# Optimization experiments

Hardware: AMD Instinct MI355X
Metric: run time of the kernel (lower is better)

Reference implementation:

```python
import jax, jax.numpy as jnp
import numpy as np

B, C, H, W = 8, 32, 256, 256


def setup_inputs() -> dict:
    key = jax.random.key(0)
    ks = jax.random.split(key, 9)
    x = jax.random.normal(ks[0], (B, C, H, W), dtype=jnp.float32)
    # depthwise 1x1 conv (groups=C) == per-channel scalar weight + bias
    def wb(kw, kb):
        w = jax.random.normal(kw, (C,), dtype=jnp.float32) * (1.0 / jnp.sqrt(1.0))
        b = jax.random.normal(kb, (C,), dtype=jnp.float32) * 0.1
        return w, b
    w_up, b_up = wb(ks[1], ks[2])
    w_right, b_right = wb(ks[3], ks[4])
    w_down, b_down = wb(ks[5], ks[6])
    w_left, b_left = wb(ks[7], ks[8])
    return {"x": x, "w_up": w_up, "b_up": b_up, "w_right": w_right,
            "b_right": b_right, "w_down": w_down, "b_down": b_down,
            "w_left": w_left, "b_left": b_left}


def _dir_scan(x_seq, w, b):
    """x_seq: [L, B, C, K]. h[0]=x[0]; h[t+1]=relu(w_c*h[t]+b_c+x[t+1])."""
    wb_ = w[None, :, None]
    bb_ = b[None, :, None]

    def step(h, xt):
        hn = jax.nn.relu(h * wb_ + bb_ + xt)
        return hn, hn

    _, ys = jax.lax.scan(step, x_seq[0], x_seq[1:])
    return jnp.concatenate([x_seq[:1], ys], axis=0)


def reference(x, w_up, b_up, w_right, b_right, w_down, b_down, w_left, b_left):
    xh = jnp.moveaxis(x, 2, 0)  # [H, B, C, W] for row scans
    xw = jnp.moveaxis(x, 3, 0)  # [W, B, C, H] for column scans

    top_down = jnp.moveaxis(_dir_scan(xh, w_down, b_down), 0, 2)
    top_up = jnp.moveaxis(_dir_scan(xh[::-1], w_up, b_up)[::-1], 0, 2)
    top_right = jnp.moveaxis(_dir_scan(xw, w_right, b_right), 0, 3)
    top_left = jnp.moveaxis(_dir_scan(xw[::-1], w_left, b_left)[::-1], 0, 3)

    return (top_up, top_right, top_down, top_left)
```

## Files before the change

### kernel.cpp

```cpp
#include <hip/hip_runtime.h>

#define BB 8
#define CC 32
#define HH 256
#define WW 256

__device__ __forceinline__ float step_v8(float h, float w, float b, float x) {
    float t = __fadd_rn(__fadd_rn(__fmul_rn(h, w), b), x);
    float r;
    asm volatile(
        "v_max_f32 %0, %1, 0\n\t"
        "v_min_f32 %0, %0, %2"
        : "=&v"(r)
        : "v"(t), "v"(3.3895313892515355e+38f));
    return r;
}

__global__ __launch_bounds__(256, 4) void irnn_fused_v8(
    const float* __restrict__ x,
    const float* __restrict__ w_up,    const float* __restrict__ b_up,
    const float* __restrict__ w_right, const float* __restrict__ b_right,
    const float* __restrict__ w_down,  const float* __restrict__ b_down,
    const float* __restrict__ w_left,  const float* __restrict__ b_left,
    float* __restrict__ out_up, float* __restrict__ out_right,
    float* __restrict__ out_down, float* __restrict__ out_left)
{
    __shared__ float tile[128 * 67];

    const int bid = blockIdx.x;
    if (bid < BB * CC) {
        const int bc   = bid;
        const int c    = bc & (CC - 1);
        const int down = (threadIdx.x < 128);
        const int t    = threadIdx.x & 127;
        const int w2   = t * 2;
        const float wc = down ? w_down[c] : w_up[c];
        const float bv = down ? b_down[c] : b_up[c];

        const long long base = (long long)bc * (HH * WW) + w2;
        const long long st   = down ? WW : -WW;
        const long long off0 = down ? 0 : (long long)(HH - 1) * WW;
        const float* xs = x + base + off0;
        float*       os = (down ? out_down : out_up) + base + off0;

        float2 h = *(const float2*)xs;
        *(float2*)os = h;

        float2 buf[8];
        #pragma unroll
        for (int i = 0; i < 8; ++i) buf[i] = *(const float2*)(xs + (1 + i) * st);

        int kb = 1;
        #pragma unroll 1
        for (int g = 0; g < 30; ++g) {
            float2 nb[8];
            #pragma unroll
            for (int i = 0; i < 8; ++i) nb[i] = *(const float2*)(xs + (kb + 8 + i) * st);
            #pragma unroll
            for (int i = 0; i < 8; ++i) {
                h.x = step_v8(h.x, wc, bv, buf[i].x);
                h.y = step_v8(h.y, wc, bv, buf[i].y);
                *(float2*)(os + (kb + i) * st) = h;
            }
            #pragma unroll
            for (int i = 0; i < 8; ++i) buf[i] = nb[i];
            kb += 8;
        }
        float2 tb[7];
        #pragma unroll
        for (int i = 0; i < 7; ++i) tb[i] = *(const float2*)(xs + (249 + i) * st);
        #pragma unroll
        for (int i = 0; i < 8; ++i) {
            h.x = step_v8(h.x, wc, bv, buf[i].x);
            h.y = step_v8(h.y, wc, bv, buf[i].y);
            *(float2*)(os + (241 + i) * st) = h;
        }
        #pragma unroll
        for (int i = 0; i < 7; ++i) {
            h.x = step_v8(h.x, wc, bv, tb[i].x);
            h.y = step_v8(h.y, wc, bv, tb[i].y);
            *(float2*)(os + (249 + i) * st) = h;
        }
        return;
    }

    const int hb  = bid - BB * CC;
    const int dir = hb & 1;
    const int rg  = hb >> 1;
    const int tid = threadIdx.x;
    const long long R0 = (long long)rg * 128;
    const int c = (int)((R0 >> 8) & (CC - 1));
    const float wc = dir ? w_left[c] : w_right[c];
    const float bv = dir ? b_left[c] : b_right[c];
    const float* xbase = x + R0 * WW;
    float* obase = (dir ? out_left : out_right) + R0 * WW;

    float h = 0.0f;
    for (int s = 0; s < 4; ++s) {
        const int tt = dir ? (3 - s) : s;
        const int w0 = tt * 64;

        #pragma unroll
        for (int it = 0; it < 8; ++it) {
            int idx = it * 256 + tid;
            int row = idx >> 4;
            int l   = idx & 15;
            float4 v = *(const float4*)(xbase + row * WW + w0 + l * 4);
            int a = row * 67 + l * 4;
            tile[a]     = v.x;
            tile[a + 1] = v.y;
            tile[a + 2] = v.z;
            tile[a + 3] = v.w;
        }
        __syncthreads();

        if (tid < 128) {
            float* trow = &tile[tid * 67];
            if (dir == 0) {
                float rb[16];
                #pragma unroll
                for (int i = 0; i < 16; ++i) rb[i] = trow[i];
                #pragma unroll
                for (int q = 0; q < 4; ++q) {
                    float nb[16];
                    if (q < 3) {
                        #pragma unroll
                        for (int i = 0; i < 16; ++i) nb[i] = trow[16 * (q + 1) + i];
                    }
                    #pragma unroll
                    for (int i = 0; i < 16; ++i) {
                        if (s == 0 && q == 0 && i == 0) h = rb[0];
                        else h = step_v8(h, wc, bv, rb[i]);
                        trow[16 * q + i] = h;
                    }
                    if (q < 3) {
                        #pragma unroll
                        for (int i = 0; i < 16; ++i) rb[i] = nb[i];
                    }
                }
            } else {
                float rb[16];
                #pragma unroll
                for (int i = 0; i < 16; ++i) rb[i] = trow[48 + i];
                #pragma unroll
                for (int q = 3; q >= 0; --q) {
                    float nb[16];
                    if (q > 0) {
                        #pragma unroll
                        for (int i = 0; i < 16; ++i) nb[i] = trow[16 * (q - 1) + i];
                    }
                    #pragma unroll
                    for (int i = 15; i >= 0; --i) {
                        if (s == 0 && q == 3 && i == 15) h = rb[15];
                        else h = step_v8(h, wc, bv, rb[i]);
                        trow[16 * q + i] = h;
                    }
                    if (q > 0) {
                        #pragma unroll
                        for (int i = 0; i < 16; ++i) rb[i] = nb[i];
                    }
                }
            }
        }
        __syncthreads();

        #pragma unroll
        for (int it = 0; it < 8; ++it) {
            int idx = it * 256 + tid;
            int row = idx >> 4;
            int l   = idx & 15;
            int a = row * 67 + l * 4;
            float4 v = make_float4(tile[a], tile[a + 1], tile[a + 2], tile[a + 3]);
            *(float4*)(obase + row * WW + w0 + l * 4) = v;
        }
        __syncthreads();
    }
}

extern "C" void kernel_launch(void* const* d_in, const int* in_sizes, int n_in,
                              void* d_out, int out_size, void* d_ws, size_t ws_size,
                              hipStream_t stream) {
    const float* x       = (const float*)d_in[0];
    const float* w_up    = (const float*)d_in[1];
    const float* b_up    = (const float*)d_in[2];
    const float* w_right = (const float*)d_in[3];
    const float* b_right = (const float*)d_in[4];
    const float* w_down  = (const float*)d_in[5];
    const float* b_down  = (const float*)d_in[6];
    const float* w_left  = (const float*)d_in[7];
    const float* b_left  = (const float*)d_in[8];

    float* out = (float*)d_out;
    const long long N = (long long)BB * CC * HH * WW;
    float* out_up    = out;
    float* out_right = out + N;
    float* out_down  = out + 2 * N;
    float* out_left  = out + 3 * N;

    irnn_fused_v8<<<dim3(BB * CC + 1024), 256, 0, stream>>>(
        x, w_up, b_up, w_right, b_right, w_down, b_down, w_left, b_left,
        out_up, out_right, out_down, out_left);
}
```

Measured before the change: 339.3 us.

## Restructure row-scan blocks with register-prefetch pipeline, interleaved roles, and nontemporal stores

Row-scan blocks now handle a whole 256-row image each, with all 256 threads scanning, in 8 column tiles of width 32. The next tile's global loads are prefetched into registers while the current tile is scanned, which removes one barrier per tile. Blocks are interleaved so column and row roles for the same (b,c) plane are launched adjacently in a 768-block grid. The step becomes an FMA plus a single med3 clamp instead of mul/add/add/max/min, and outputs use nontemporal stores. This trades larger per-block work and changed rounding (fma) for fewer blocks and less barrier overhead.

```diff
diff --git a/kernel.cpp b/kernel.cpp
--- a/kernel.cpp
+++ b/kernel.cpp
@@ -5,18 +5,21 @@
 #define HH 256
 #define WW 256
 
-__device__ __forceinline__ float step_v8(float h, float w, float b, float x) {
-    float t = __fadd_rn(__fadd_rn(__fmul_rn(h, w), b), x);
+typedef float vf2 __attribute__((ext_vector_type(2)));
+typedef float vf4 __attribute__((ext_vector_type(4)));
+
+__device__ __forceinline__ float step_v9(float h, float w, float bx) {
+    float t = __fmaf_rn(h, w, bx);
     float r;
-    asm volatile(
-        "v_max_f32 %0, %1, 0\n\t"
-        "v_min_f32 %0, %0, %2"
-        : "=&v"(r)
-        : "v"(t), "v"(3.3895313892515355e+38f));
+    asm volatile("v_med3_f32 %0, %1, 0, %2"
+                 : "=v"(r)
+                 : "v"(t), "v"(3.3895313892515355e+38f));
     return r;
 }
 
-__global__ __launch_bounds__(256, 4) void irnn_fused_v8(
+#define LDS_BARRIER() asm volatile("s_waitcnt lgkmcnt(0)\n\ts_barrier" ::: "memory")
+
+__global__ __launch_bounds__(256, 4) void irnn_fused_v9(
     const float* __restrict__ x,
     const float* __restrict__ w_up,    const float* __restrict__ b_up,
     const float* __restrict__ w_right, const float* __restrict__ b_right,
@@ -25,12 +28,17 @@
     float* __restrict__ out_up, float* __restrict__ out_right,
     float* __restrict__ out_down, float* __restrict__ out_left)
 {
-    __shared__ float tile[128 * 67];
-
-    const int bid = blockIdx.x;
-    if (bid < BB * CC) {
-        const int bc   = bid;
-        const int c    = bc & (CC - 1);
+    __shared__ float tile[256 * 33];
+
+    const int p    = blockIdx.x;
+    const int x8   = p & 7;
+    const int slot = p >> 3;
+    const int pg   = slot / 3;
+    const int role = slot - pg * 3;
+    const int bc   = pg * 8 + x8;
+    const int c    = bc & (CC - 1);
+
+    if (role == 0) {
         const int down = (threadIdx.x < 128);
         const int t    = threadIdx.x & 127;
         const int w2   = t * 2;
@@ -43,137 +51,151 @@
         const float* xs = x + base + off0;
         float*       os = (down ? out_down : out_up) + base + off0;
 
-        float2 h = *(const float2*)xs;
-        *(float2*)os = h;
-
-        float2 buf[8];
-        #pragma unroll
-        for (int i = 0; i < 8; ++i) buf[i] = *(const float2*)(xs + (1 + i) * st);
+        vf2 h = *(const vf2*)xs;
+        __builtin_nontemporal_store(h, (vf2*)os);
+
+        vf2 buf[8];
+        #pragma unroll
+        for (int i = 0; i < 8; ++i) buf[i] = *(const vf2*)(xs + (1 + i) * st);
 
         int kb = 1;
         #pragma unroll 1
         for (int g = 0; g < 30; ++g) {
-            float2 nb[8];
-            #pragma unroll
-            for (int i = 0; i < 8; ++i) nb[i] = *(const float2*)(xs + (kb + 8 + i) * st);
+            vf2 nb[8];
+            #pragma unroll
+            for (int i = 0; i < 8; ++i) nb[i] = *(const vf2*)(xs + (kb + 8 + i) * st);
             #pragma unroll
             for (int i = 0; i < 8; ++i) {
-                h.x = step_v8(h.x, wc, bv, buf[i].x);
-                h.y = step_v8(h.y, wc, bv, buf[i].y);
-                *(float2*)(os + (kb + i) * st) = h;
+                h.x = step_v9(h.x, wc, __fadd_rn(bv, buf[i].x));
+                h.y = step_v9(h.y, wc, __fadd_rn(bv, buf[i].y));
+                __builtin_nontemporal_store(h, (vf2*)(os + (kb + i) * st));
             }
             #pragma unroll
             for (int i = 0; i < 8; ++i) buf[i] = nb[i];
             kb += 8;
         }
-        float2 tb[7];
-        #pragma unroll
-        for (int i = 0; i < 7; ++i) tb[i] = *(const float2*)(xs + (249 + i) * st);
+        vf2 tb[7];
+        #pragma unroll
+        for (int i = 0; i < 7; ++i) tb[i] = *(const vf2*)(xs + (249 + i) * st);
         #pragma unroll
         for (int i = 0; i < 8; ++i) {
-            h.x = step_v8(h.x, wc, bv, buf[i].x);
-            h.y = step_v8(h.y, wc, bv, buf[i].y);
-            *(float2*)(os + (241 + i) * st) = h;
+            h.x = step_v9(h.x, wc, __fadd_rn(bv, buf[i].x));
+            h.y = step_v9(h.y, wc, __fadd_rn(bv, buf[i].y));
+            __builtin_nontemporal_store(h, (vf2*)(os + (241 + i) * st));
         }
         #pragma unroll
         for (int i = 0; i < 7; ++i) {
-            h.x = step_v8(h.x, wc, bv, tb[i].x);
-            h.y = step_v8(h.y, wc, bv, tb[i].y);
-            *(float2*)(os + (249 + i) * st) = h;
+            h.x = step_v9(h.x, wc, __fadd_rn(bv, tb[i].x));
+            h.y = step_v9(h.y, wc, __fadd_rn(bv, tb[i].y));
+            __builtin_nontemporal_store(h, (vf2*)(os + (249 + i) * st));
         }
         return;
     }
 
-    const int hb  = bid - BB * CC;
-    const int dir = hb & 1;
-    const int rg  = hb >> 1;
+    const int dir = role - 1;
     const int tid = threadIdx.x;
-    const long long R0 = (long long)rg * 128;
-    const int c = (int)((R0 >> 8) & (CC - 1));
     const float wc = dir ? w_left[c] : w_right[c];
     const float bv = dir ? b_left[c] : b_right[c];
-    const float* xbase = x + R0 * WW;
-    float* obase = (dir ? out_left : out_right) + R0 * WW;
-
-    float h = 0.0f;
-    for (int s = 0; s < 4; ++s) {
-        const int tt = dir ? (3 - s) : s;
-        const int w0 = tt * 64;
-
+    const float* xbase = x + (long long)bc * (HH * WW);
+    float* obase = (dir ? out_left : out_right) + (long long)bc * (HH * WW);
+
+    vf4 st4[8];
+
+    {
+        const int w0 = dir ? (7 * 32) : 0;
         #pragma unroll
         for (int it = 0; it < 8; ++it) {
             int idx = it * 256 + tid;
-            int row = idx >> 4;
-            int l   = idx & 15;
-            float4 v = *(const float4*)(xbase + row * WW + w0 + l * 4);
-            int a = row * 67 + l * 4;
-            tile[a]     = v.x;
-            tile[a + 1] = v.y;
-            tile[a + 2] = v.z;
-            tile[a + 3] = v.w;
-        }
-        __syncthreads();
-
-        if (tid < 128) {
-            float* trow = &tile[tid * 67];
+            int row = idx >> 3, l = idx & 7;
+            st4[it] = *(const vf4*)(xbase + row * WW + w0 + l * 4);
+        }
+        #pragma unroll
+        for (int it = 0; it < 8; ++it) {
+            int idx = it * 256 + tid;
+            int row = idx >> 3, l = idx & 7;
+            int a = row * 33 + l * 4;
+            tile[a]     = st4[it].x;
+            tile[a + 1] = st4[it].y;
+            tile[a + 2] = st4[it].z;
+            tile[a + 3] = st4[it].w;
+        }
+    }
+    LDS_BARRIER();
+
+    float h = 0.0f;
+    float* trow = &tile[tid * 33];
+    #pragma unroll 1
+    for (int s = 0; s < 8; ++s) {
+        const int cur = dir ? (7 - s) : s;
+        const int w0c = cur * 32;
+
+        if (s < 7) {
+            const int nw0 = (dir ? (6 - s) : (s + 1)) * 32;
+            #pragma unroll
+            for (int it = 0; it < 8; ++it) {
+                int idx = it * 256 + tid;
+                int row = idx >> 3, l = idx & 7;
+                st4[it] = *(const vf4*)(xbase + row * WW + nw0 + l * 4);
+            }
+        }
+
+        {
+            float rb[32];
+            #pragma unroll
+            for (int i = 0; i < 32; ++i) rb[i] = trow[i];
             if (dir == 0) {
-                float rb[16];
-                #pragma unroll
-                for (int i = 0; i < 16; ++i) rb[i] = trow[i];
-                #pragma unroll
-                for (int q = 0; q < 4; ++q) {
-                    float nb[16];
-                    if (q < 3) {
-                        #pragma unroll
-                        for (int i = 0; i < 16; ++i) nb[i] = trow[16 * (q + 1) + i];
-                    }
-                    #pragma unroll
-                    for (int i = 0; i < 16; ++i) {
-                        if (s == 0 && q == 0 && i == 0) h = rb[0];
-                        else h = step_v8(h, wc, bv, rb[i]);
-                        trow[16 * q + i] = h;
-                    }
-                    if (q < 3) {
-                        #pragma unroll
-                        for (int i = 0; i < 16; ++i) rb[i] = nb[i];
+                if (s == 0) {
+                    h = rb[0]; trow[0] = h;
+                    #pragma unroll
+                    for (int i = 1; i < 32; ++i) {
+                        h = step_v9(h, wc, __fadd_rn(bv, rb[i]));
+                        trow[i] = h;
+                    }
+                } else {
+                    #pragma unroll
+                    for (int i = 0; i < 32; ++i) {
+                        h = step_v9(h, wc, __fadd_rn(bv, rb[i]));
+                        trow[i] = h;
                     }
                 }
             } else {
-                float rb[16];
-                #pragma unroll
-                for (int i = 0; i < 16; ++i) rb[i] = trow[48 + i];
-                #pragma unroll
-                for (int q = 3; q >= 0; --q) {
-                    float nb[16];
-                    if (q > 0) {
-                        #pragma unroll
-                        for (int i = 0; i < 16; ++i) nb[i] = trow[16 * (q - 1) + i];
-                    }
-                    #pragma unroll
-                    for (int i = 15; i >= 0; --i) {
-                        if (s == 0 && q == 3 && i == 15) h = rb[15];
-                        else h = step_v8(h, wc, bv, rb[i]);
-                        trow[16 * q + i] = h;
-                    }
-                    if (q > 0) {
-                        #pragma unroll
-                        for (int i = 0; i < 16; ++i) rb[i] = nb[i];
+                if (s == 0) {
+                    h = rb[31]; trow[31] = h;
+                    #pragma unroll
+                    for (int i = 30; i >= 0; --i) {
+                        h = step_v9(h, wc, __fadd_rn(bv, rb[i]));
+                        trow[i] = h;
+                    }
+                } else {
+                    #pragma unroll
+                    for (int i = 31; i >= 0; --i) {
+                        h = step_v9(h, wc, __fadd_rn(bv, rb[i]));
+                        trow[i] = h;
                     }
                 }
             }
         }
-        __syncthreads();
+        LDS_BARRIER();
 
         #pragma unroll
         for (int it = 0; it < 8; ++it) {
             int idx = it * 256 + tid;
-            int row = idx >> 4;
-            int l   = idx & 15;
-            int a = row * 67 + l * 4;
-            float4 v = make_float4(tile[a], tile[a + 1], tile[a + 2], tile[a + 3]);
-            *(float4*)(obase + row * WW + w0 + l * 4) = v;
-        }
-        __syncthreads();
+            int row = idx >> 3, l = idx & 7;
+            int a = row * 33 + l * 4;
+            vf4 v;
+            v.x = tile[a];
+            v.y = tile[a + 1];
+            v.z = tile[a + 2];
+            v.w = tile[a + 3];
+            __builtin_nontemporal_store(v, (vf4*)(obase + row * WW + w0c + l * 4));
+            if (s < 7) {
+                tile[a]     = st4[it].x;
+                tile[a + 1] = st4[it].y;
+                tile[a + 2] = st4[it].z;
+                tile[a + 3] = st4[it].w;
+            }
+        }
+        LDS_BARRIER();
     }
 }
 
@@ -197,7 +219,7 @@
     float* out_down  = out + 2 * N;
     float* out_left  = out + 3 * N;
 
-    irnn_fused_v8<<<dim3(BB * CC + 1024), 256, 0, stream>>>(
+    irnn_fused_v9<<<dim3(768), 256, 0, stream>>>(
         x, w_up, b_up, w_right, b_right, w_down, b_down, w_left, b_left,
         out_up, out_right, out_down, out_left);
 }
```

After: 333.9 us. About the same (-1.6%).
